# Performance work log

Measured on AMD Instinct MI355X. Metric: run time of the kernel, lower is better.

The kernel has to match this reference:

```python
import jax, jax.numpy as jnp
import numpy as np

VOCAB, D_WORD, D_TOPIC, D_NOUN_HIDDEN = 50000, 300, 128, 312
B, L = 8192, 32
N_MONTH = D_NOUN_HIDDEN - D_WORD  # 12


def setup_inputs() -> dict:
    key = jax.random.key(0)
    ks = jax.random.split(key, 8)
    return {
        "topic_emb": jax.random.normal(ks[0], (D_TOPIC,), dtype=jnp.float32),
        "noun_ids": jax.random.randint(ks[1], (B, L), 0, VOCAB),
        "lengths": jax.random.randint(ks[2], (B,), 0, 33),
        "months": jax.random.randint(ks[3], (B,), 0, N_MONTH),
        "month_info_encode": 1,
        "we": jax.random.normal(ks[4], (VOCAB, D_WORD), dtype=jnp.float32),
        "k_w": jax.random.normal(ks[5], (D_TOPIC, D_NOUN_HIDDEN), dtype=jnp.float32) * (1.0 / np.sqrt(D_NOUN_HIDDEN)),
        "k_b": jnp.zeros((D_TOPIC,), dtype=jnp.float32),
        "q_w": jax.random.normal(ks[6], (D_TOPIC, D_TOPIC), dtype=jnp.float32) * (1.0 / np.sqrt(D_TOPIC)),
        "q_b": jnp.zeros((D_TOPIC,), dtype=jnp.float32),
    }


def reference(topic_emb, noun_ids, lengths, months, month_info_encode, we, k_w, k_b, q_w, q_b):
    # Ragged per-sample loop collapsed into one padded+masked batch pass.
    Bn, Ln = noun_ids.shape
    d_topic = q_w.shape[0]
    emb = we[noun_ids]  # [B, L, d_word] embedding lookup
    # one-hot month features, broadcast over tokens: [B, L, N_MONTH]
    month_oh = jax.nn.one_hot(months, N_MONTH, dtype=emb.dtype) * jnp.asarray(month_info_encode, emb.dtype)
    month_part = jnp.broadcast_to(month_oh[:, None, :], (Bn, Ln, N_MONTH))
    value = jnp.concatenate([emb, month_part], axis=-1)  # [B, L, Dh]
    key = value @ k_w.T + k_b                            # [B, L, d_topic]
    query = topic_emb @ q_w.T + q_b                      # [d_topic]
    scale = 1.0 / jnp.sqrt(jnp.asarray(d_topic, value.dtype))
    scores = jnp.einsum('bld,d->bl', key, query) * scale  # [B, L]
    valid = jnp.arange(Ln)[None, :] < lengths[:, None]    # ragged mask
    attn = jax.nn.softmax(jnp.where(valid, scores, -1e9), axis=-1)
    out = jnp.einsum('bl,bld->bd', attn, value)           # [B, Dh]
    # samples with empty spans stay zero (original leaves outputs[i] = 0)
    return jnp.where((lengths > 0)[:, None], out, jnp.zeros_like(out))
```

## Files before the change

kernel.cpp:

```cpp
#include <hip/hip_runtime.h>
#include <math.h>

#define VOCAB 50000
#define D_WORD 300
#define D_TOPIC 128
#define DH 312
#define NB 8192
#define LMAX 32
#define N_MONTH 12

__global__ __launch_bounds__(320) void compute_w_kernel(
    const float* __restrict__ topic_emb,
    const float* __restrict__ q_w, const float* __restrict__ q_b,
    const float* __restrict__ k_w,
    float* __restrict__ w_out)
{
    __shared__ float query_s[D_TOPIC];
    int t = threadIdx.x;
    if (t < D_TOPIC) {
        float q = q_b[t];
        for (int k = 0; k < D_TOPIC; ++k)
            q = fmaf(q_w[t * D_TOPIC + k], topic_emb[k], q);
        query_s[t] = q;
    }
    __syncthreads();
    if (t < DH) {
        float acc = 0.f;
        for (int d = 0; d < D_TOPIC; ++d)
            acc = fmaf(k_w[d * DH + t], query_s[d], acc);
        w_out[t] = acc;
    }
}

__global__ __launch_bounds__(256) void vocab_score_kernel(
    const float* __restrict__ we, const float* __restrict__ w,
    float* __restrict__ s_vocab)
{
    __shared__ float4 w4[75];
    int t = threadIdx.x;
    if (t < 75) w4[t] = ((const float4*)w)[t];
    __syncthreads();
    int wave = t >> 6, lane = t & 63;
    int row = blockIdx.x * 4 + wave;
    if (row >= VOCAB) return;
    const float4* r = (const float4*)(we + (size_t)row * D_WORD);
    float4 a = r[lane];
    float4 ww = w4[lane];
    float p = fmaf(a.x, ww.x, fmaf(a.y, ww.y, fmaf(a.z, ww.z, a.w * ww.w)));
    if (lane < 11) {
        float4 b = r[64 + lane];
        float4 wb = w4[64 + lane];
        p = fmaf(b.x, wb.x, fmaf(b.y, wb.y, fmaf(b.z, wb.z, fmaf(b.w, wb.w, p))));
    }
    #pragma unroll
    for (int off = 32; off > 0; off >>= 1)
        p += __shfl_xor(p, off);
    if (lane == 0) s_vocab[row] = p;
}

__global__ __launch_bounds__(256) void attn_kernel(
    const int* __restrict__ noun_ids, const int* __restrict__ lengths,
    const int* __restrict__ months, const int* __restrict__ encode_p,
    const float* __restrict__ we, const float* __restrict__ s_vocab,
    float* __restrict__ out)
{
    int wave = threadIdx.x >> 6, lane = threadIdx.x & 63;
    int b = blockIdx.x * 4 + wave;
    float4* ob = (float4*)(out + (size_t)b * DH);
    int len = lengths[b];

    if (len <= 0) {
        float4 z = {0.f, 0.f, 0.f, 0.f};
        ob[lane] = z;
        if (lane < 14) ob[64 + lane] = z;
        return;
    }
    if (len > LMAX) len = LMAX;

    int id = 0;
    float sc = -INFINITY;
    if (lane < LMAX) {
        id = noun_ids[b * LMAX + lane];
        if (lane < len) sc = s_vocab[id] * 0.08838834764831845f;
    }
    float m = sc;
    #pragma unroll
    for (int off = 32; off > 0; off >>= 1) m = fmaxf(m, __shfl_xor(m, off));
    float e = (lane < len) ? __expf(sc - m) : 0.f;
    float s = e;
    #pragma unroll
    for (int off = 32; off > 0; off >>= 1) s += __shfl_xor(s, off);
    float rs = 1.f / s;

    float4 acc0 = {0.f, 0.f, 0.f, 0.f};
    float4 acc1 = {0.f, 0.f, 0.f, 0.f};
    for (int l = 0; l < len; ++l) {
        float a = __shfl(e, l) * rs;
        int rid = __shfl(id, l);
        const float4* r = (const float4*)(we + (size_t)rid * D_WORD);
        float4 v = r[lane];
        acc0.x = fmaf(a, v.x, acc0.x);
        acc0.y = fmaf(a, v.y, acc0.y);
        acc0.z = fmaf(a, v.z, acc0.z);
        acc0.w = fmaf(a, v.w, acc0.w);
        if (lane < 11) {
            float4 v1 = r[64 + lane];
            acc1.x = fmaf(a, v1.x, acc1.x);
            acc1.y = fmaf(a, v1.y, acc1.y);
            acc1.z = fmaf(a, v1.z, acc1.z);
            acc1.w = fmaf(a, v1.w, acc1.w);
        }
    }
    ob[lane] = acc0;
    if (lane < 11) {
        ob[64 + lane] = acc1;
    } else if (lane < 14) {
        int mo = months[b];
        float enc = (float)(*encode_p);
        int base = (lane - 11) * 4;
        float4 oh;
        oh.x = (base + 0 == mo) ? enc : 0.f;
        oh.y = (base + 1 == mo) ? enc : 0.f;
        oh.z = (base + 2 == mo) ? enc : 0.f;
        oh.w = (base + 3 == mo) ? enc : 0.f;
        ob[64 + lane] = oh;
    }
}

extern "C" void kernel_launch(void* const* d_in, const int* in_sizes, int n_in,
                              void* d_out, int out_size, void* d_ws, size_t ws_size,
                              hipStream_t stream) {
    const float* topic_emb = (const float*)d_in[0];
    const int*   noun_ids  = (const int*)d_in[1];
    const int*   lengths   = (const int*)d_in[2];
    const int*   months    = (const int*)d_in[3];
    const int*   encode    = (const int*)d_in[4];
    const float* we        = (const float*)d_in[5];
    const float* k_w       = (const float*)d_in[6];
    const float* q_w       = (const float*)d_in[8];
    const float* q_b       = (const float*)d_in[9];
    float* out = (float*)d_out;

    float* w_vec   = (float*)d_ws;
    float* s_vocab = w_vec + 512;

    compute_w_kernel<<<1, 320, 0, stream>>>(topic_emb, q_w, q_b, k_w, w_vec);
    vocab_score_kernel<<<(VOCAB + 3) / 4, 256, 0, stream>>>(we, w_vec, s_vocab);
    attn_kernel<<<NB / 4, 256, 0, stream>>>(noun_ids, lengths, months, encode,
                                            we, s_vocab, out);
}
```

Baseline: 148.5 us.

## Split each sample's token loop across two waves and combine via shared memory

The attention kernel now assigns two waves per sample, each gathering and accumulating half of the token rows, with the second wave's partial sums reduced through shared memory before the first wave writes the output. The grid doubles to keep one sample per wave pair. This is meant to expose more memory-level parallelism for the latency-bound embedding gathers. The softmax scale is folded into the vocab score kernel. The cost is a block-wide barrier, duplicated softmax work in both waves, and LDS traffic.

```diff
diff --git a/kernel.cpp b/kernel.cpp
--- a/kernel.cpp
+++ b/kernel.cpp
@@ -55,7 +55,7 @@
     #pragma unroll
     for (int off = 32; off > 0; off >>= 1)
         p += __shfl_xor(p, off);
-    if (lane == 0) s_vocab[row] = p;
+    if (lane == 0) s_vocab[row] = p * 0.08838834764831845f;
 }
 
 __global__ __launch_bounds__(256) void attn_kernel(
@@ -64,66 +64,82 @@
     const float* __restrict__ we, const float* __restrict__ s_vocab,
     float* __restrict__ out)
 {
+    __shared__ float4 part[2][76];
     int wave = threadIdx.x >> 6, lane = threadIdx.x & 63;
-    int b = blockIdx.x * 4 + wave;
-    float4* ob = (float4*)(out + (size_t)b * DH);
+    int pair = wave >> 1, half = wave & 1;
+    int b = blockIdx.x * 2 + pair;
     int len = lengths[b];
-
-    if (len <= 0) {
-        float4 z = {0.f, 0.f, 0.f, 0.f};
-        ob[lane] = z;
-        if (lane < 14) ob[64 + lane] = z;
-        return;
-    }
     if (len > LMAX) len = LMAX;
-
-    int id = 0;
-    float sc = -INFINITY;
-    if (lane < LMAX) {
-        id = noun_ids[b * LMAX + lane];
-        if (lane < len) sc = s_vocab[id] * 0.08838834764831845f;
-    }
-    float m = sc;
-    #pragma unroll
-    for (int off = 32; off > 0; off >>= 1) m = fmaxf(m, __shfl_xor(m, off));
-    float e = (lane < len) ? __expf(sc - m) : 0.f;
-    float s = e;
-    #pragma unroll
-    for (int off = 32; off > 0; off >>= 1) s += __shfl_xor(s, off);
-    float rs = 1.f / s;
+    bool valid = (len > 0);
 
     float4 acc0 = {0.f, 0.f, 0.f, 0.f};
     float4 acc1 = {0.f, 0.f, 0.f, 0.f};
-    for (int l = 0; l < len; ++l) {
-        float a = __shfl(e, l) * rs;
-        int rid = __shfl(id, l);
-        const float4* r = (const float4*)(we + (size_t)rid * D_WORD);
-        float4 v = r[lane];
-        acc0.x = fmaf(a, v.x, acc0.x);
-        acc0.y = fmaf(a, v.y, acc0.y);
-        acc0.z = fmaf(a, v.z, acc0.z);
-        acc0.w = fmaf(a, v.w, acc0.w);
-        if (lane < 11) {
-            float4 v1 = r[64 + lane];
-            acc1.x = fmaf(a, v1.x, acc1.x);
-            acc1.y = fmaf(a, v1.y, acc1.y);
-            acc1.z = fmaf(a, v1.z, acc1.z);
-            acc1.w = fmaf(a, v1.w, acc1.w);
+    float p = 0.f;
+    int id = 0;
+
+    if (valid) {
+        float sc = -INFINITY;
+        if (lane < LMAX) {
+            id = noun_ids[b * LMAX + lane];
+            if (lane < len) sc = s_vocab[id];
+        }
+        float m = sc;
+        #pragma unroll
+        for (int off = 32; off > 0; off >>= 1) m = fmaxf(m, __shfl_xor(m, off));
+        float e = (lane < len) ? __expf(sc - m) : 0.f;
+        float s = e;
+        #pragma unroll
+        for (int off = 32; off > 0; off >>= 1) s += __shfl_xor(s, off);
+        p = e * (1.f / s);
+
+        int h  = (len + 1) >> 1;
+        int l0 = half ? h : 0;
+        int l1 = half ? len : h;
+        for (int l = l0; l < l1; ++l) {
+            float a  = __shfl(p, l);
+            int  rid = __shfl(id, l);
+            const float4* r = (const float4*)(we + (size_t)rid * D_WORD);
+            float4 v = r[lane];
+            acc0.x = fmaf(a, v.x, acc0.x);
+            acc0.y = fmaf(a, v.y, acc0.y);
+            acc0.z = fmaf(a, v.z, acc0.z);
+            acc0.w = fmaf(a, v.w, acc0.w);
+            if (lane < 11) {
+                float4 v1 = r[64 + lane];
+                acc1.x = fmaf(a, v1.x, acc1.x);
+                acc1.y = fmaf(a, v1.y, acc1.y);
+                acc1.z = fmaf(a, v1.z, acc1.z);
+                acc1.w = fmaf(a, v1.w, acc1.w);
+            }
         }
     }
-    ob[lane] = acc0;
-    if (lane < 11) {
-        ob[64 + lane] = acc1;
-    } else if (lane < 14) {
-        int mo = months[b];
-        float enc = (float)(*encode_p);
-        int base = (lane - 11) * 4;
-        float4 oh;
-        oh.x = (base + 0 == mo) ? enc : 0.f;
-        oh.y = (base + 1 == mo) ? enc : 0.f;
-        oh.z = (base + 2 == mo) ? enc : 0.f;
-        oh.w = (base + 3 == mo) ? enc : 0.f;
-        ob[64 + lane] = oh;
+
+    if (half == 1) {
+        part[pair][lane] = acc0;
+        if (lane < 11) part[pair][64 + lane] = acc1;
+    }
+    __syncthreads();
+
+    if (half == 0) {
+        float4* ob = (float4*)(out + (size_t)b * DH);
+        float4 q0 = part[pair][lane];
+        acc0.x += q0.x; acc0.y += q0.y; acc0.z += q0.z; acc0.w += q0.w;
+        ob[lane] = acc0;
+        if (lane < 11) {
+            float4 q1 = part[pair][64 + lane];
+            acc1.x += q1.x; acc1.y += q1.y; acc1.z += q1.z; acc1.w += q1.w;
+            ob[64 + lane] = acc1;
+        } else if (lane < 14) {
+            int mo = months[b];
+            float enc = valid ? (float)(*encode_p) : 0.f;
+            int base = (lane - 11) * 4;
+            float4 oh;
+            oh.x = (base + 0 == mo) ? enc : 0.f;
+            oh.y = (base + 1 == mo) ? enc : 0.f;
+            oh.z = (base + 2 == mo) ? enc : 0.f;
+            oh.w = (base + 3 == mo) ? enc : 0.f;
+            ob[64 + lane] = oh;
+        }
     }
 }
 
@@ -146,6 +162,6 @@
 
     compute_w_kernel<<<1, 320, 0, stream>>>(topic_emb, q_w, q_b, k_w, w_vec);
     vocab_score_kernel<<<(VOCAB + 3) / 4, 256, 0, stream>>>(we, w_vec, s_vocab);
-    attn_kernel<<<NB / 4, 256, 0, stream>>>(noun_ids, lengths, months, encode,
+    attn_kernel<<<NB / 2, 256, 0, stream>>>(noun_ids, lengths, months, encode,
                                             we, s_vocab, out);
 }
```

After: 148.8 us. Within noise of the previous version (+0.2%).

## Fuse vocab scoring into attention with online softmax over gathered rows

Applied to the files above, without the earlier changes.

Drops the pass that scores all 50000 vocabulary rows and instead computes each token's score inside the attention kernel from the embedding row it already gathers. The softmax becomes an online running max with rescaled accumulators, and the scale factor is folded into w. This avoids reading the whole embedding table (about 60 MB) to score it, at the cost of a serial cross-lane reduction and two exps per token inside the gather loop.

```diff
diff --git a/kernel.cpp b/kernel.cpp
--- a/kernel.cpp
+++ b/kernel.cpp
@@ -28,40 +28,14 @@
         float acc = 0.f;
         for (int d = 0; d < D_TOPIC; ++d)
             acc = fmaf(k_w[d * DH + t], query_s[d], acc);
-        w_out[t] = acc;
+        w_out[t] = acc * 0.08838834764831845f;
     }
 }
 
-__global__ __launch_bounds__(256) void vocab_score_kernel(
-    const float* __restrict__ we, const float* __restrict__ w,
-    float* __restrict__ s_vocab)
-{
-    __shared__ float4 w4[75];
-    int t = threadIdx.x;
-    if (t < 75) w4[t] = ((const float4*)w)[t];
-    __syncthreads();
-    int wave = t >> 6, lane = t & 63;
-    int row = blockIdx.x * 4 + wave;
-    if (row >= VOCAB) return;
-    const float4* r = (const float4*)(we + (size_t)row * D_WORD);
-    float4 a = r[lane];
-    float4 ww = w4[lane];
-    float p = fmaf(a.x, ww.x, fmaf(a.y, ww.y, fmaf(a.z, ww.z, a.w * ww.w)));
-    if (lane < 11) {
-        float4 b = r[64 + lane];
-        float4 wb = w4[64 + lane];
-        p = fmaf(b.x, wb.x, fmaf(b.y, wb.y, fmaf(b.z, wb.z, fmaf(b.w, wb.w, p))));
-    }
-    #pragma unroll
-    for (int off = 32; off > 0; off >>= 1)
-        p += __shfl_xor(p, off);
-    if (lane == 0) s_vocab[row] = p;
-}
-
-__global__ __launch_bounds__(256) void attn_kernel(
+__global__ __launch_bounds__(256) void attn_fused_kernel(
     const int* __restrict__ noun_ids, const int* __restrict__ lengths,
     const int* __restrict__ months, const int* __restrict__ encode_p,
-    const float* __restrict__ we, const float* __restrict__ s_vocab,
+    const float* __restrict__ we, const float* __restrict__ w,
     float* __restrict__ out)
 {
     int wave = threadIdx.x >> 6, lane = threadIdx.x & 63;
@@ -77,42 +51,48 @@
     }
     if (len > LMAX) len = LMAX;
 
-    int id = 0;
-    float sc = -INFINITY;
-    if (lane < LMAX) {
-        id = noun_ids[b * LMAX + lane];
-        if (lane < len) sc = s_vocab[id] * 0.08838834764831845f;
-    }
-    float m = sc;
-    #pragma unroll
-    for (int off = 32; off > 0; off >>= 1) m = fmaxf(m, __shfl_xor(m, off));
-    float e = (lane < len) ? __expf(sc - m) : 0.f;
-    float s = e;
-    #pragma unroll
-    for (int off = 32; off > 0; off >>= 1) s += __shfl_xor(s, off);
-    float rs = 1.f / s;
+    const float4* w4 = (const float4*)w;
+    float4 ww = w4[lane];
+    float4 wb = (lane < 11) ? w4[64 + lane] : (float4){0.f, 0.f, 0.f, 0.f};
 
+    int id = (lane < LMAX) ? noun_ids[b * LMAX + lane] : 0;
+
+    float m = -1e30f, denom = 0.f;
     float4 acc0 = {0.f, 0.f, 0.f, 0.f};
     float4 acc1 = {0.f, 0.f, 0.f, 0.f};
+
     for (int l = 0; l < len; ++l) {
-        float a = __shfl(e, l) * rs;
         int rid = __shfl(id, l);
         const float4* r = (const float4*)(we + (size_t)rid * D_WORD);
-        float4 v = r[lane];
-        acc0.x = fmaf(a, v.x, acc0.x);
-        acc0.y = fmaf(a, v.y, acc0.y);
-        acc0.z = fmaf(a, v.z, acc0.z);
-        acc0.w = fmaf(a, v.w, acc0.w);
-        if (lane < 11) {
-            float4 v1 = r[64 + lane];
-            acc1.x = fmaf(a, v1.x, acc1.x);
-            acc1.y = fmaf(a, v1.y, acc1.y);
-            acc1.z = fmaf(a, v1.z, acc1.z);
-            acc1.w = fmaf(a, v1.w, acc1.w);
-        }
+        float4 v0 = r[lane];
+        float4 v1 = (lane < 11) ? r[64 + lane] : (float4){0.f, 0.f, 0.f, 0.f};
+        float p = fmaf(v0.x, ww.x, fmaf(v0.y, ww.y,
+                  fmaf(v0.z, ww.z, fmaf(v0.w, ww.w,
+                  fmaf(v1.x, wb.x, fmaf(v1.y, wb.y,
+                  fmaf(v1.z, wb.z, v1.w * wb.w)))))));
+        #pragma unroll
+        for (int off = 32; off > 0; off >>= 1)
+            p += __shfl_xor(p, off);
+        float mn = fmaxf(m, p);
+        float c  = __expf(m - mn);
+        float e  = __expf(p - mn);
+        m = mn;
+        denom = fmaf(denom, c, e);
+        acc0.x = fmaf(acc0.x, c, e * v0.x);
+        acc0.y = fmaf(acc0.y, c, e * v0.y);
+        acc0.z = fmaf(acc0.z, c, e * v0.z);
+        acc0.w = fmaf(acc0.w, c, e * v0.w);
+        acc1.x = fmaf(acc1.x, c, e * v1.x);
+        acc1.y = fmaf(acc1.y, c, e * v1.y);
+        acc1.z = fmaf(acc1.z, c, e * v1.z);
+        acc1.w = fmaf(acc1.w, c, e * v1.w);
     }
+
+    float rs = 1.f / denom;
+    acc0.x *= rs; acc0.y *= rs; acc0.z *= rs; acc0.w *= rs;
     ob[lane] = acc0;
     if (lane < 11) {
+        acc1.x *= rs; acc1.y *= rs; acc1.z *= rs; acc1.w *= rs;
         ob[64 + lane] = acc1;
     } else if (lane < 14) {
         int mo = months[b];
@@ -141,11 +121,9 @@
     const float* q_b       = (const float*)d_in[9];
     float* out = (float*)d_out;
 
-    float* w_vec   = (float*)d_ws;
-    float* s_vocab = w_vec + 512;
+    float* w_vec = (float*)d_ws;
 
     compute_w_kernel<<<1, 320, 0, stream>>>(topic_emb, q_w, q_b, k_w, w_vec);
-    vocab_score_kernel<<<(VOCAB + 3) / 4, 256, 0, stream>>>(we, w_vec, s_vocab);
-    attn_kernel<<<NB / 4, 256, 0, stream>>>(noun_ids, lengths, months, encode,
-                                            we, s_vocab, out);
+    attn_fused_kernel<<<NB / 4, 256, 0, stream>>>(noun_ids, lengths, months,
+                                                  encode, we, w_vec, out);
 }
```

New measurement: 138.9 us. -6.5%, faster.
